# Kernel optimization log

Measured on AMD Instinct MI355X. Metric: run time of the kernel, lower is better.

## Reference

```python
import jax, jax.numpy as jnp
import numpy as np
from jax import lax

MAX_ITERS = 64
SDF_EPS = 0.0001
N_RAYS = 1048576
HIDDEN = 128


def setup_inputs() -> dict:
    key = jax.random.key(0)
    ks = jax.random.split(key, 8)
    # Camera-ish rays: origins on a shell at z=-3, directions aimed at the unit sphere at the origin
    origins = jax.random.normal(ks[0], (N_RAYS, 3), dtype=jnp.float32) * 0.05 + jnp.array([0.0, 0.0, -3.0], jnp.float32)
    noise = jax.random.normal(ks[1], (N_RAYS, 3), dtype=jnp.float32) * 0.2
    d = -origins + noise
    directions = d / jnp.linalg.norm(d, axis=-1, keepdims=True)
    # Learnable analytic sphere SDF params
    center = jnp.zeros((3,), jnp.float32)
    radius = jnp.array(1.0, jnp.float32)
    # Color MLP params (get_color): 3 -> HIDDEN -> 3
    W1 = jax.random.normal(ks[2], (3, HIDDEN), dtype=jnp.float32) * (1.0 / np.sqrt(3.0))
    b1 = jnp.zeros((HIDDEN,), jnp.float32)
    W2 = jax.random.normal(ks[3], (HIDDEN, 3), dtype=jnp.float32) * (1.0 / np.sqrt(HIDDEN))
    b2 = jnp.zeros((3,), jnp.float32)
    return {"origins": origins, "directions": directions, "center": center,
            "radius": radius, "W1": W1, "b1": b1, "W2": W2, "b2": b2}


def _sdf(points, center, radius):
    # [N,3] -> [N,1]
    return jnp.linalg.norm(points - center, axis=-1, keepdims=True) - radius


def reference(origins, directions, center, radius, W1, b1, W2, b2):
    # Sphere tracing: sdf is evaluated, THEN points are advanced; final mask uses
    # the sdf from the last iteration (pre-update), matching the torch loop.
    def step(pts, _):
        sdf = _sdf(pts, center, radius)
        return pts + sdf * directions, sdf

    points, sdfs = lax.scan(step, origins, None, length=MAX_ITERS)
    mask = sdfs[-1] < SDF_EPS  # [N,1]

    # get_color on intersection points; scatter into zeros elsewhere
    h = jax.nn.relu(points @ W1 + b1)          # [N, HIDDEN]
    col = jax.nn.sigmoid(h @ W2 + b2)          # [N, 3]
    color = jnp.where(mask, col, jnp.zeros_like(col))
    return color
```

## Files before the change

### kernel.cpp

```cpp
#include <hip/hip_runtime.h>
#include <math.h>

#define BLOCK 256
#define NRPT 4
#define HIDDEN_ 128
#define MAXIT 64

typedef float v2f __attribute__((ext_vector_type(2)));

__device__ __forceinline__ v2f ld2(const float* p) {
    return *reinterpret_cast<const v2f*>(p);
}

template<int H>
__device__ __forceinline__ v2f pk_mul_b(v2f a, v2f b) {
    v2f d;
    if constexpr (H == 0)
        asm("v_pk_mul_f32 %0, %1, %2 op_sel:[0,0] op_sel_hi:[1,0]"
            : "=v"(d) : "v"(a), "s"(b));
    else
        asm("v_pk_mul_f32 %0, %1, %2 op_sel:[0,1] op_sel_hi:[1,1]"
            : "=v"(d) : "v"(a), "s"(b));
    return d;
}
template<int H>
__device__ __forceinline__ v2f pk_fma_b(v2f a, v2f b, v2f c) {
    v2f d;
    if constexpr (H == 0)
        asm("v_pk_fma_f32 %0, %1, %2, %3 op_sel:[0,0,0] op_sel_hi:[1,0,1]"
            : "=v"(d) : "v"(a), "s"(b), "v"(c));
    else
        asm("v_pk_fma_f32 %0, %1, %2, %3 op_sel:[0,1,0] op_sel_hi:[1,1,1]"
            : "=v"(d) : "v"(a), "s"(b), "v"(c));
    return d;
}
template<int H>
__device__ __forceinline__ v2f pk_add_b(v2f a, v2f b) {
    v2f d;
    if constexpr (H == 0)
        asm("v_pk_add_f32 %0, %1, %2 op_sel:[0,0] op_sel_hi:[1,0]"
            : "=v"(d) : "v"(a), "s"(b));
    else
        asm("v_pk_add_f32 %0, %1, %2 op_sel:[0,1] op_sel_hi:[1,1]"
            : "=v"(d) : "v"(a), "s"(b));
    return d;
}
__device__ __forceinline__ v2f pk_relu(v2f a) {
    v2f d;
    d.x = fmaxf(a.x, 0.0f);
    d.y = fmaxf(a.y, 0.0f);
    return d;
}

__global__ __launch_bounds__(BLOCK) void sphere_trace_kernel(
    const float* __restrict__ origins,
    const float* __restrict__ directions,
    const float* __restrict__ center,
    const float* __restrict__ radius,
    const float* __restrict__ W1,
    const float* __restrict__ b1,
    const float* __restrict__ W2,
    const float* __restrict__ b2,
    float* __restrict__ out,
    int nray)
{
    const float cx = center[0], cy = center[1], cz = center[2];
    const float rad = radius[0];
    const float bo0 = b2[0], bo1 = b2[1], bo2 = b2[2];

    const int tid = threadIdx.x;
    const int base = (blockIdx.x * BLOCK + tid) * NRPT;
    if (base >= nray) return;

    const float4* o4 = reinterpret_cast<const float4*>(origins + 3 * (size_t)base);
    const float4* d4 = reinterpret_cast<const float4*>(directions + 3 * (size_t)base);
    const float4 oA = o4[0], oB = o4[1], oC = o4[2];
    const float4 dA = d4[0], dB = d4[1], dC = d4[2];

    float qx[NRPT], qy[NRPT], qz[NRPT];
    float dx[NRPT], dy[NRPT], dz[NRPT];

    qx[0] = oA.x - cx; qy[0] = oA.y - cy; qz[0] = oA.z - cz;
    qx[1] = oA.w - cx; qy[1] = oB.x - cy; qz[1] = oB.y - cz;
    qx[2] = oB.z - cx; qy[2] = oB.w - cy; qz[2] = oC.x - cz;
    qx[3] = oC.y - cx; qy[3] = oC.z - cy; qz[3] = oC.w - cz;

    dx[0] = dA.x; dy[0] = dA.y; dz[0] = dA.z;
    dx[1] = dA.w; dy[1] = dB.x; dz[1] = dB.y;
    dx[2] = dB.z; dy[2] = dB.w; dz[2] = dC.x;
    dx[3] = dC.y; dy[3] = dC.z; dz[3] = dC.w;

    float slast[NRPT], sprev[NRPT];
#pragma unroll
    for (int r = 0; r < NRPT; ++r) { slast[r] = 0.0f; sprev[r] = INFINITY; }

    for (int ob = 0; ob < MAXIT / 4; ++ob) {
#pragma unroll
        for (int ii = 0; ii < 4; ++ii) {
#pragma unroll
            for (int r = 0; r < NRPT; ++r) {
                float f = qx[r] * qx[r];
                f = fmaf(qy[r], qy[r], f);
                f = fmaf(qz[r], qz[r], f);
                const float s = __builtin_amdgcn_sqrtf(f) - rad;
                qx[r] = fmaf(s, dx[r], qx[r]);
                qy[r] = fmaf(s, dy[r], qy[r]);
                qz[r] = fmaf(s, dz[r], qz[r]);
                slast[r] = s;
            }
        }
        bool done = true;
#pragma unroll
        for (int r = 0; r < NRPT; ++r) {
            const float s = slast[r];
            const bool conv = s < 1e-5f;
            const bool dead = (s >= sprev[r]) && (s > 1e-3f);
            done = done && (conv || dead || !(s == s));
            sprev[r] = s;
        }
        if (__all(done)) break;
    }

    v2f pxp[2], pyp[2], pzp[2];
    pxp[0] = v2f{qx[0] + cx, qx[1] + cx};
    pyp[0] = v2f{qy[0] + cy, qy[1] + cy};
    pzp[0] = v2f{qz[0] + cz, qz[1] + cz};
    pxp[1] = v2f{qx[2] + cx, qx[3] + cx};
    pyp[1] = v2f{qy[2] + cy, qy[3] + cy};
    pzp[1] = v2f{qz[2] + cz, qz[3] + cz};

    v2f a0p[2], a1p[2], a2p[2];
    a0p[0] = v2f{bo0, bo0}; a1p[0] = v2f{bo1, bo1}; a2p[0] = v2f{bo2, bo2};
    a0p[1] = a0p[0];        a1p[1] = a1p[0];        a2p[1] = a2p[0];

#pragma unroll 4
    for (int j = 0; j < HIDDEN_; j += 2) {
        const v2f w0p = ld2(W1 + j);
        const v2f w1p = ld2(W1 + HIDDEN_ + j);
        const v2f w2p = ld2(W1 + 2 * HIDDEN_ + j);
        const v2f bbp = ld2(b1 + j);
        const v2f Ap  = ld2(W2 + 3 * j);
        const v2f Bp  = ld2(W2 + 3 * j + 2);
        const v2f Cp  = ld2(W2 + 3 * j + 4);
#pragma unroll
        for (int pr = 0; pr < 2; ++pr) {
            v2f t0 = pk_mul_b<0>(pxp[pr], w0p);
            t0 = pk_fma_b<0>(pyp[pr], w1p, t0);
            t0 = pk_fma_b<0>(pzp[pr], w2p, t0);
            const v2f hj = pk_relu(pk_add_b<0>(t0, bbp));

            v2f t1 = pk_mul_b<1>(pxp[pr], w0p);
            t1 = pk_fma_b<1>(pyp[pr], w1p, t1);
            t1 = pk_fma_b<1>(pzp[pr], w2p, t1);
            const v2f hj1 = pk_relu(pk_add_b<1>(t1, bbp));

            a0p[pr] = pk_fma_b<0>(hj, Ap, a0p[pr]);
            a1p[pr] = pk_fma_b<1>(hj, Ap, a1p[pr]);
            a2p[pr] = pk_fma_b<0>(hj, Bp, a2p[pr]);
            a0p[pr] = pk_fma_b<1>(hj1, Bp, a0p[pr]);
            a1p[pr] = pk_fma_b<0>(hj1, Cp, a1p[pr]);
            a2p[pr] = pk_fma_b<1>(hj1, Cp, a2p[pr]);
        }
    }

    float a0[NRPT], a1[NRPT], a2[NRPT];
    a0[0] = a0p[0].x; a0[1] = a0p[0].y; a0[2] = a0p[1].x; a0[3] = a0p[1].y;
    a1[0] = a1p[0].x; a1[1] = a1p[0].y; a1[2] = a1p[1].x; a1[3] = a1p[1].y;
    a2[0] = a2p[0].x; a2[1] = a2p[0].y; a2[2] = a2p[1].x; a2[3] = a2p[1].y;

    float colv[NRPT][3];
#pragma unroll
    for (int r = 0; r < NRPT; ++r) {
        const bool hit = slast[r] < 0.0001f;
        const float c0 = __builtin_amdgcn_rcpf(1.0f + __expf(-a0[r]));
        const float c1 = __builtin_amdgcn_rcpf(1.0f + __expf(-a1[r]));
        const float c2 = __builtin_amdgcn_rcpf(1.0f + __expf(-a2[r]));
        colv[r][0] = hit ? c0 : 0.0f;
        colv[r][1] = hit ? c1 : 0.0f;
        colv[r][2] = hit ? c2 : 0.0f;
    }

    float4* ov = reinterpret_cast<float4*>(out + 3 * (size_t)base);
    ov[0] = make_float4(colv[0][0], colv[0][1], colv[0][2], colv[1][0]);
    ov[1] = make_float4(colv[1][1], colv[1][2], colv[2][0], colv[2][1]);
    ov[2] = make_float4(colv[2][2], colv[3][0], colv[3][1], colv[3][2]);
}

extern "C" void kernel_launch(void* const* d_in, const int* in_sizes, int n_in,
                              void* d_out, int out_size, void* d_ws, size_t ws_size,
                              hipStream_t stream) {
    (void)d_ws; (void)ws_size; (void)n_in; (void)out_size;
    const float* origins    = (const float*)d_in[0];
    const float* directions = (const float*)d_in[1];
    const float* center     = (const float*)d_in[2];
    const float* radius     = (const float*)d_in[3];
    const float* W1         = (const float*)d_in[4];
    const float* b1         = (const float*)d_in[5];
    const float* W2         = (const float*)d_in[6];
    const float* b2         = (const float*)d_in[7];
    float* out = (float*)d_out;

    const int nray = in_sizes[0] / 3;
    const int blocks = (nray + BLOCK * NRPT - 1) / (BLOCK * NRPT);
    sphere_trace_kernel<<<blocks, BLOCK, 0, stream>>>(
        origins, directions, center, radius, W1, b1, W2, b2, out, nray);
}
```

Measured before the change: 109.8 us.

## Solve ray-sphere intersection analytically and skip iterative tracing for clear rays

Before the sphere-tracing loop, each ray gets a closed-form ray-sphere test. Rays that clearly hit are moved straight to the analytic intersection point, and rays that clearly miss are marked as misses. The iterative loop now runs only when some lane in the wavefront holds a borderline ray, which removes most of the 64-step loop work. The cost is extra per-ray setup math, and results may differ slightly from the iterated reference near the surface and for edge cases such as unconverged grazing rays.

```diff
diff --git a/kernel.cpp b/kernel.cpp
--- a/kernel.cpp
+++ b/kernel.cpp
@@ -90,35 +90,69 @@
     dx[2] = dB.z; dy[2] = dB.w; dz[2] = dC.x;
     dx[3] = dC.y; dy[3] = dC.z; dz[3] = dC.w;
 
-    float slast[NRPT], sprev[NRPT];
-#pragma unroll
-    for (int r = 0; r < NRPT; ++r) { slast[r] = 0.0f; sprev[r] = INFINITY; }
-
-    for (int ob = 0; ob < MAXIT / 4; ++ob) {
-#pragma unroll
-        for (int ii = 0; ii < 4; ++ii) {
+    float slast[NRPT];
+    bool  slow[NRPT];
+    const float r2 = rad * rad;
+    const float thr_hit  = 0.0625f * r2;
+    const float thr_miss = -2.5e-3f * r2;
+    const float rout = (rad + 0.05f) * (rad + 0.05f);
+    bool anySlow = false;
+#pragma unroll
+    for (int r = 0; r < NRPT; ++r) {
+        float nq2 = qx[r] * qx[r];
+        nq2 = fmaf(qy[r], qy[r], nq2);
+        nq2 = fmaf(qz[r], qz[r], nq2);
+        float tc = -(qx[r] * dx[r]);
+        tc = fmaf(-qy[r], dy[r], tc);
+        tc = fmaf(-qz[r], dz[r], tc);
+        const float disc = fmaf(tc, tc, r2 - nq2);
+        const bool outside = nq2 > rout;
+        const bool fasthit = outside && (tc > 0.0f) && (disc >= thr_hit);
+        const bool fastmiss = outside && ((disc < thr_miss) || (tc <= 0.0f));
+        slow[r] = !(fasthit || fastmiss);
+        anySlow = anySlow || slow[r];
+        if (fasthit) {
+            const float tstar = tc - __builtin_amdgcn_sqrtf(disc);
+            qx[r] = fmaf(tstar, dx[r], qx[r]);
+            qy[r] = fmaf(tstar, dy[r], qy[r]);
+            qz[r] = fmaf(tstar, dz[r], qz[r]);
+        }
+        slast[r] = fasthit ? 0.0f : 1.0f;
+    }
+
+    if (__any(anySlow)) {
+        float sprev[NRPT];
+#pragma unroll
+        for (int r = 0; r < NRPT; ++r) sprev[r] = INFINITY;
+        for (int ob = 0; ob < MAXIT / 4; ++ob) {
+#pragma unroll
+            for (int ii = 0; ii < 4; ++ii) {
+#pragma unroll
+                for (int r = 0; r < NRPT; ++r) {
+                    float f = qx[r] * qx[r];
+                    f = fmaf(qy[r], qy[r], f);
+                    f = fmaf(qz[r], qz[r], f);
+                    const float s = __builtin_amdgcn_sqrtf(f) - rad;
+                    const float nx = fmaf(s, dx[r], qx[r]);
+                    const float ny = fmaf(s, dy[r], qy[r]);
+                    const float nz = fmaf(s, dz[r], qz[r]);
+                    qx[r] = slow[r] ? nx : qx[r];
+                    qy[r] = slow[r] ? ny : qy[r];
+                    qz[r] = slow[r] ? nz : qz[r];
+                    slast[r] = slow[r] ? s : slast[r];
+                }
+            }
+            bool done = true;
 #pragma unroll
             for (int r = 0; r < NRPT; ++r) {
-                float f = qx[r] * qx[r];
-                f = fmaf(qy[r], qy[r], f);
-                f = fmaf(qz[r], qz[r], f);
-                const float s = __builtin_amdgcn_sqrtf(f) - rad;
-                qx[r] = fmaf(s, dx[r], qx[r]);
-                qy[r] = fmaf(s, dy[r], qy[r]);
-                qz[r] = fmaf(s, dz[r], qz[r]);
-                slast[r] = s;
+                const float s = slast[r];
+                const bool conv = s < 1e-5f;
+                const bool dead = (s >= sprev[r]) && (s > 1e-3f);
+                done = done && (!slow[r] || conv || dead || !(s == s));
+                sprev[r] = s;
             }
+            if (__all(done)) break;
         }
-        bool done = true;
-#pragma unroll
-        for (int r = 0; r < NRPT; ++r) {
-            const float s = slast[r];
-            const bool conv = s < 1e-5f;
-            const bool dead = (s >= sprev[r]) && (s > 1e-3f);
-            done = done && (conv || dead || !(s == s));
-            sprev[r] = s;
-        }
-        if (__all(done)) break;
     }
 
     v2f pxp[2], pyp[2], pzp[2];
```

Result: no change. 109.0 us (-0.8%).
